# Performance work log

Measured on AMD Instinct MI355X. Metric: run time of the kernel, lower is better.

The kernel has to match this reference:

```python
import jax, jax.numpy as jnp
import numpy as np

PRUNE_RATIO = 0.5
MIXUP_ALPHA = 0.05


def setup_inputs() -> dict:
    key = jax.random.key(0)
    k1, k2 = jax.random.split(key)
    seq = jax.random.normal(k1, (16, 4096, 1024), dtype=jnp.float32)
    attn_weights = jax.random.normal(k2, (16, 4096), dtype=jnp.float32)
    return {"seq": seq, "attn_weights": attn_weights}


def reference(seq, attn_weights):
    # Eval-mode forward (adversarial_mix only fires in training mode).
    B, N, D = seq.shape
    k = max(1, int(N * (1.0 - PRUNE_RATIO)))  # number of kept tokens
    _, top_idx = jax.lax.top_k(attn_weights, k)  # (B, k) int32
    # gather selected tokens: (B, k, D)
    selected = jnp.take_along_axis(seq, top_idx[:, :, None], axis=1)
    # mask of pruned (non-selected) tokens: ones scattered to zero at top_idx
    batch_ids = jnp.arange(B)[:, None]
    mask = jnp.ones((B, N), dtype=seq.dtype).at[batch_ids, top_idx].set(0.0)
    # masked mean of pruned tokens, scaled by mixup_alpha -> one extra token
    rem_sum = jnp.einsum('bn,bnd->bd', mask, seq)              # (B, D)
    rem_cnt = jnp.sum(mask, axis=1, keepdims=True) + 1e-10     # (B, 1)
    rem_tok = (MIXUP_ALPHA * rem_sum / rem_cnt)[:, None, :]    # (B, 1, D)
    return jnp.concatenate([selected, rem_tok], axis=1)         # (B, k+1, D)
```

## Files before the change

### kernel.cpp

```cpp
#include <hip/hip_runtime.h>

#define BATCH 16
#define NTOK  4096
#define DIM   1024
#define KSEL  2048
#define NPRUNE 2048
#define SUM_CHUNKS 64
#define ROWS_PER_CHUNK (NPRUNE / SUM_CHUNKS)
#define COPY_ROWS 4
#define NCOPY (KSEL / COPY_ROWS)

#define NBIN 4096
#define RTHREADS 1024
#define TPT (NTOK / RTHREADS)
#define BPT (NBIN / RTHREADS)

typedef __attribute__((ext_vector_type(4))) float f32x4;

__global__ __launch_bounds__(1024) void rank_kernel(
    const float* __restrict__ w, int* __restrict__ sel, int* __restrict__ pr) {
  __shared__ unsigned int s_cnt[NBIN];
  __shared__ unsigned int s_base[NBIN];
  __shared__ unsigned int s_cur[NBIN];
  __shared__ unsigned long long s_key[NTOK];
  __shared__ unsigned int s_wsum[16];
  __shared__ unsigned int s_woff[16];

  const int b = blockIdx.x;
  const int t = threadIdx.x;
  const float* wb = w + (size_t)b * NTOK;

  for (int i = t; i < NBIN; i += RTHREADS) s_cnt[i] = 0;
  __syncthreads();

  unsigned int inv[TPT];
  unsigned int bin[TPT];
  int tok[TPT];
#pragma unroll
  for (int p = 0; p < TPT; ++p) {
    const int j = p * RTHREADS + t;
    const unsigned int u = __float_as_uint(wb[j]);
    const unsigned int s = (u & 0x80000000u) ? ~u : (u | 0x80000000u);
    const unsigned int iv = ~s;
    inv[p] = iv; tok[p] = j; bin[p] = iv >> 20;
    atomicAdd(&s_cnt[bin[p]], 1u);
  }
  __syncthreads();

  unsigned int c[BPT];
  unsigned int lsum = 0;
#pragma unroll
  for (int i = 0; i < BPT; ++i) { c[i] = s_cnt[t * BPT + i]; lsum += c[i]; }
  const int lane = t & 63, wid = t >> 6;
  unsigned int v = lsum;
  for (int d = 1; d < 64; d <<= 1) {
    unsigned int up = __shfl_up(v, d, 64);
    if (lane >= d) v += up;
  }
  if (lane == 63) s_wsum[wid] = v;
  __syncthreads();
  if (t == 0) {
    unsigned int run = 0;
    for (int i = 0; i < 16; ++i) { const unsigned int x = s_wsum[i]; s_woff[i] = run; run += x; }
  }
  __syncthreads();
  unsigned int excl = v - lsum + s_woff[wid];
#pragma unroll
  for (int i = 0; i < BPT; ++i) {
    s_base[t * BPT + i] = excl;
    s_cur[t * BPT + i] = excl;
    excl += c[i];
  }
  __syncthreads();

  unsigned long long key[TPT];
#pragma unroll
  for (int p = 0; p < TPT; ++p) {
    key[p] = ((unsigned long long)inv[p] << 32) | (unsigned int)tok[p];
    const unsigned int pos = atomicAdd(&s_cur[bin[p]], 1u);
    s_key[pos] = key[p];
  }
  __syncthreads();

  int* selb = sel + b * KSEL;
  int* prb  = pr + b * NPRUNE;
#pragma unroll
  for (int p = 0; p < TPT; ++p) {
    const unsigned int bb = bin[p];
    const unsigned int st = s_base[bb];
    const unsigned int en = s_cur[bb];
    unsigned int r = st;
    for (unsigned int q = st; q < en; ++q) r += (s_key[q] < key[p]);
    if (r < KSEL) selb[r] = tok[p];
    else          prb[r - KSEL] = tok[p];
  }
}

__global__ __launch_bounds__(256) void gather_partial_kernel(
    const float* __restrict__ seq, const int* __restrict__ sel,
    const int* __restrict__ pr, float* __restrict__ out,
    float* __restrict__ part) {
  const int b = blockIdx.y;
  const int t = blockIdx.x;
  const f32x4* seqb = (const f32x4*)(seq + (size_t)b * NTOK * DIM);
  const int lane = threadIdx.x;

  if (t < SUM_CHUNKS) {
    const int* prb = pr + b * NPRUNE + t * ROWS_PER_CHUNK;
    f32x4 a0 = {0.f, 0.f, 0.f, 0.f}, a1 = a0, a2 = a0, a3 = a0;
#pragma unroll
    for (int r = 0; r < ROWS_PER_CHUNK; r += 4) {
      const int r0 = prb[r + 0], r1 = prb[r + 1];
      const int r2 = prb[r + 2], r3 = prb[r + 3];
      const f32x4 x0 = __builtin_nontemporal_load(seqb + (size_t)r0 * (DIM / 4) + lane);
      const f32x4 x1 = __builtin_nontemporal_load(seqb + (size_t)r1 * (DIM / 4) + lane);
      const f32x4 x2 = __builtin_nontemporal_load(seqb + (size_t)r2 * (DIM / 4) + lane);
      const f32x4 x3 = __builtin_nontemporal_load(seqb + (size_t)r3 * (DIM / 4) + lane);
      a0 += x0; a1 += x1; a2 += x2; a3 += x3;
    }
    const f32x4 acc = (a0 + a1) + (a2 + a3);
    f32x4* pdst = (f32x4*)(part + ((size_t)b * SUM_CHUNKS + t) * DIM);
    pdst[lane] = acc;
  } else {
    const int c = t - SUM_CHUNKS;
    const int base = c * COPY_ROWS;
    const int* selb = sel + b * KSEL + base;
    const int i0 = selb[0], i1 = selb[1], i2 = selb[2], i3 = selb[3];
    const f32x4 x0 = __builtin_nontemporal_load(seqb + (size_t)i0 * (DIM / 4) + lane);
    const f32x4 x1 = __builtin_nontemporal_load(seqb + (size_t)i1 * (DIM / 4) + lane);
    const f32x4 x2 = __builtin_nontemporal_load(seqb + (size_t)i2 * (DIM / 4) + lane);
    const f32x4 x3 = __builtin_nontemporal_load(seqb + (size_t)i3 * (DIM / 4) + lane);
    f32x4* dst = (f32x4*)(out + (size_t)b * (KSEL + 1) * DIM +
                          (size_t)base * DIM);
    __builtin_nontemporal_store(x0, dst + 0 * (DIM / 4) + lane);
    __builtin_nontemporal_store(x1, dst + 1 * (DIM / 4) + lane);
    __builtin_nontemporal_store(x2, dst + 2 * (DIM / 4) + lane);
    __builtin_nontemporal_store(x3, dst + 3 * (DIM / 4) + lane);
  }
}

__global__ __launch_bounds__(256) void reduce_kernel(
    const float* __restrict__ part, float* __restrict__ out, float scale) {
  __shared__ f32x4 s_acc[4][64];
  const int b = blockIdx.y, qq = blockIdx.x;
  const int t = threadIdx.x, g = t >> 6, col = t & 63;
  const int c4 = qq * 64 + col;
  const f32x4* p = (const f32x4*)(part + (size_t)b * SUM_CHUNKS * DIM);
  f32x4 acc = {0.f, 0.f, 0.f, 0.f};
#pragma unroll
  for (int i = 0; i < SUM_CHUNKS / 4; ++i) {
    const int ch = g + 4 * i;
    acc += p[(size_t)ch * (DIM / 4) + c4];
  }
  s_acc[g][col] = acc;
  __syncthreads();
  if (g == 0) {
    f32x4 r = (s_acc[0][col] + s_acc[1][col]) + (s_acc[2][col] + s_acc[3][col]);
    r *= scale;
    f32x4* dst = (f32x4*)(out + (size_t)b * (KSEL + 1) * DIM +
                          (size_t)KSEL * DIM);
    dst[c4] = r;
  }
}

extern "C" void kernel_launch(void* const* d_in, const int* in_sizes, int n_in,
                              void* d_out, int out_size, void* d_ws, size_t ws_size,
                              hipStream_t stream) {
  (void)in_sizes; (void)n_in; (void)out_size; (void)ws_size;
  const float* seq = (const float*)d_in[0];
  const float* w   = (const float*)d_in[1];
  float* out = (float*)d_out;

  int* sel = (int*)d_ws;
  int* pr  = sel + BATCH * KSEL;
  float* part = (float*)(pr + BATCH * NPRUNE);

  rank_kernel<<<BATCH, RTHREADS, 0, stream>>>(w, sel, pr);
  gather_partial_kernel<<<dim3(SUM_CHUNKS + NCOPY, BATCH), 256, 0, stream>>>(
      seq, sel, pr, out, part);
  const float scale = (float)(0.05 / (2048.0 + 1e-10));
  reduce_kernel<<<dim3(4, BATCH), 256, 0, stream>>>(part, out, scale);
}
```

Baseline: 414.8 us.

## Stream seq rows contiguously using per-token ranks instead of index gathers

The rank kernel now writes a per-token rank array and is split across 4 blocks per batch. Each block rebuilds the histogram and then ranks only its quarter of the tokens, which spreads the serial rank-counting work. The gather kernel reads each batch's seq rows sequentially. Each row is scattered to its output slot if its rank is below k, otherwise it is added to a partial sum, so reads are contiguous instead of index-driven gathers. The trade-offs are redundant histogram work in the rank kernel, per-row branch divergence on the rank test, and 128 partial sums per batch for the reduce kernel instead of 64.

```diff
diff --git a/kernel.cpp b/kernel.cpp
--- a/kernel.cpp
+++ b/kernel.cpp
@@ -5,20 +5,20 @@
 #define DIM   1024
 #define KSEL  2048
 #define NPRUNE 2048
-#define SUM_CHUNKS 64
-#define ROWS_PER_CHUNK (NPRUNE / SUM_CHUNKS)
-#define COPY_ROWS 4
-#define NCOPY (KSEL / COPY_ROWS)
 
 #define NBIN 4096
 #define RTHREADS 1024
+#define RBLK 4
 #define TPT (NTOK / RTHREADS)
 #define BPT (NBIN / RTHREADS)
+
+#define GROWS 32
+#define GBLK (NTOK / GROWS)
 
 typedef __attribute__((ext_vector_type(4))) float f32x4;
 
 __global__ __launch_bounds__(1024) void rank_kernel(
-    const float* __restrict__ w, int* __restrict__ sel, int* __restrict__ pr) {
+    const float* __restrict__ w, int* __restrict__ rk) {
   __shared__ unsigned int s_cnt[NBIN];
   __shared__ unsigned int s_base[NBIN];
   __shared__ unsigned int s_cur[NBIN];
@@ -26,7 +26,8 @@
   __shared__ unsigned int s_wsum[16];
   __shared__ unsigned int s_woff[16];
 
-  const int b = blockIdx.x;
+  const int b = blockIdx.y;
+  const int qq = blockIdx.x;
   const int t = threadIdx.x;
   const float* wb = w + (size_t)b * NTOK;
 
@@ -35,14 +36,13 @@
 
   unsigned int inv[TPT];
   unsigned int bin[TPT];
-  int tok[TPT];
 #pragma unroll
   for (int p = 0; p < TPT; ++p) {
     const int j = p * RTHREADS + t;
     const unsigned int u = __float_as_uint(wb[j]);
     const unsigned int s = (u & 0x80000000u) ? ~u : (u | 0x80000000u);
     const unsigned int iv = ~s;
-    inv[p] = iv; tok[p] = j; bin[p] = iv >> 20;
+    inv[p] = iv; bin[p] = iv >> 20;
     atomicAdd(&s_cnt[bin[p]], 1u);
   }
   __syncthreads();
@@ -73,70 +73,52 @@
   }
   __syncthreads();
 
-  unsigned long long key[TPT];
 #pragma unroll
   for (int p = 0; p < TPT; ++p) {
-    key[p] = ((unsigned long long)inv[p] << 32) | (unsigned int)tok[p];
+    const int j = p * RTHREADS + t;
+    const unsigned long long key =
+        ((unsigned long long)inv[p] << 32) | (unsigned int)j;
     const unsigned int pos = atomicAdd(&s_cur[bin[p]], 1u);
-    s_key[pos] = key[p];
+    s_key[pos] = key;
   }
   __syncthreads();
 
-  int* selb = sel + b * KSEL;
-  int* prb  = pr + b * NPRUNE;
-#pragma unroll
-  for (int p = 0; p < TPT; ++p) {
-    const unsigned int bb = bin[p];
-    const unsigned int st = s_base[bb];
-    const unsigned int en = s_cur[bb];
-    unsigned int r = st;
-    for (unsigned int q = st; q < en; ++q) r += (s_key[q] < key[p]);
-    if (r < KSEL) selb[r] = tok[p];
-    else          prb[r - KSEL] = tok[p];
-  }
+  const int tok = qq * RTHREADS + t;
+  const unsigned int u = __float_as_uint(wb[tok]);
+  const unsigned int s = (u & 0x80000000u) ? ~u : (u | 0x80000000u);
+  const unsigned int iv = ~s;
+  const unsigned long long key =
+      ((unsigned long long)iv << 32) | (unsigned int)tok;
+  const unsigned int bb = iv >> 20;
+  const unsigned int st = s_base[bb];
+  const unsigned int en = s_cur[bb];
+  unsigned int r = st;
+  for (unsigned int q = st; q < en; ++q) r += (s_key[q] < key);
+  rk[b * NTOK + tok] = (int)r;
 }
 
-__global__ __launch_bounds__(256) void gather_partial_kernel(
-    const float* __restrict__ seq, const int* __restrict__ sel,
-    const int* __restrict__ pr, float* __restrict__ out,
-    float* __restrict__ part) {
-  const int b = blockIdx.y;
-  const int t = blockIdx.x;
-  const f32x4* seqb = (const f32x4*)(seq + (size_t)b * NTOK * DIM);
+__global__ __launch_bounds__(256) void gather_kernel(
+    const float* __restrict__ seq, const int* __restrict__ rk,
+    float* __restrict__ out, float* __restrict__ part) {
+  const int b = blockIdx.y, g = blockIdx.x;
   const int lane = threadIdx.x;
-
-  if (t < SUM_CHUNKS) {
-    const int* prb = pr + b * NPRUNE + t * ROWS_PER_CHUNK;
-    f32x4 a0 = {0.f, 0.f, 0.f, 0.f}, a1 = a0, a2 = a0, a3 = a0;
-#pragma unroll
-    for (int r = 0; r < ROWS_PER_CHUNK; r += 4) {
-      const int r0 = prb[r + 0], r1 = prb[r + 1];
-      const int r2 = prb[r + 2], r3 = prb[r + 3];
-      const f32x4 x0 = __builtin_nontemporal_load(seqb + (size_t)r0 * (DIM / 4) + lane);
-      const f32x4 x1 = __builtin_nontemporal_load(seqb + (size_t)r1 * (DIM / 4) + lane);
-      const f32x4 x2 = __builtin_nontemporal_load(seqb + (size_t)r2 * (DIM / 4) + lane);
-      const f32x4 x3 = __builtin_nontemporal_load(seqb + (size_t)r3 * (DIM / 4) + lane);
-      a0 += x0; a1 += x1; a2 += x2; a3 += x3;
+  const f32x4* src = (const f32x4*)(seq + (size_t)b * NTOK * DIM) +
+                     (size_t)g * GROWS * (DIM / 4);
+  const int* rkb = rk + b * NTOK + g * GROWS;
+  f32x4* outb = (f32x4*)(out + (size_t)b * (KSEL + 1) * DIM);
+  f32x4 acc = {0.f, 0.f, 0.f, 0.f};
+#pragma unroll 8
+  for (int i = 0; i < GROWS; ++i) {
+    const f32x4 x = __builtin_nontemporal_load(src + (size_t)i * (DIM / 4) + lane);
+    const int r = rkb[i];
+    if (r < KSEL) {
+      __builtin_nontemporal_store(x, outb + (size_t)r * (DIM / 4) + lane);
+    } else {
+      acc += x;
     }
-    const f32x4 acc = (a0 + a1) + (a2 + a3);
-    f32x4* pdst = (f32x4*)(part + ((size_t)b * SUM_CHUNKS + t) * DIM);
-    pdst[lane] = acc;
-  } else {
-    const int c = t - SUM_CHUNKS;
-    const int base = c * COPY_ROWS;
-    const int* selb = sel + b * KSEL + base;
-    const int i0 = selb[0], i1 = selb[1], i2 = selb[2], i3 = selb[3];
-    const f32x4 x0 = __builtin_nontemporal_load(seqb + (size_t)i0 * (DIM / 4) + lane);
-    const f32x4 x1 = __builtin_nontemporal_load(seqb + (size_t)i1 * (DIM / 4) + lane);
-    const f32x4 x2 = __builtin_nontemporal_load(seqb + (size_t)i2 * (DIM / 4) + lane);
-    const f32x4 x3 = __builtin_nontemporal_load(seqb + (size_t)i3 * (DIM / 4) + lane);
-    f32x4* dst = (f32x4*)(out + (size_t)b * (KSEL + 1) * DIM +
-                          (size_t)base * DIM);
-    __builtin_nontemporal_store(x0, dst + 0 * (DIM / 4) + lane);
-    __builtin_nontemporal_store(x1, dst + 1 * (DIM / 4) + lane);
-    __builtin_nontemporal_store(x2, dst + 2 * (DIM / 4) + lane);
-    __builtin_nontemporal_store(x3, dst + 3 * (DIM / 4) + lane);
   }
+  f32x4* pdst = (f32x4*)(part + ((size_t)b * GBLK + g) * DIM);
+  pdst[lane] = acc;
 }
 
 __global__ __launch_bounds__(256) void reduce_kernel(
@@ -145,10 +127,10 @@
   const int b = blockIdx.y, qq = blockIdx.x;
   const int t = threadIdx.x, g = t >> 6, col = t & 63;
   const int c4 = qq * 64 + col;
-  const f32x4* p = (const f32x4*)(part + (size_t)b * SUM_CHUNKS * DIM);
+  const f32x4* p = (const f32x4*)(part + (size_t)b * GBLK * DIM);
   f32x4 acc = {0.f, 0.f, 0.f, 0.f};
 #pragma unroll
-  for (int i = 0; i < SUM_CHUNKS / 4; ++i) {
+  for (int i = 0; i < GBLK / 4; ++i) {
     const int ch = g + 4 * i;
     acc += p[(size_t)ch * (DIM / 4) + c4];
   }
@@ -171,13 +153,11 @@
   const float* w   = (const float*)d_in[1];
   float* out = (float*)d_out;
 
-  int* sel = (int*)d_ws;
-  int* pr  = sel + BATCH * KSEL;
-  float* part = (float*)(pr + BATCH * NPRUNE);
+  int* rk = (int*)d_ws;
+  float* part = (float*)(rk + BATCH * NTOK);
 
-  rank_kernel<<<BATCH, RTHREADS, 0, stream>>>(w, sel, pr);
-  gather_partial_kernel<<<dim3(SUM_CHUNKS + NCOPY, BATCH), 256, 0, stream>>>(
-      seq, sel, pr, out, part);
+  rank_kernel<<<dim3(RBLK, BATCH), RTHREADS, 0, stream>>>(w, rk);
+  gather_kernel<<<dim3(GBLK, BATCH), 256, 0, stream>>>(seq, rk, out, part);
   const float scale = (float)(0.05 / (2048.0 + 1e-10));
   reduce_kernel<<<dim3(4, BATCH), 256, 0, stream>>>(part, out, scale);
 }
```

Result: faster. 404.9 us (-2.4%).
